# Kernel tuning notes

Measured on AMD Instinct MI355X. Metric: run time of the kernel, lower is better.

## Reference

```python
import jax, jax.numpy as jnp
import numpy as np

# Model dims (match init_kwargs)
B, S, D = 4, 2048, 1024          # batch, seq, d_model
H, E, DH = 8, 4, 128             # n_heads, n_experts_attn, d_head
K = 2                            # k_attn (routed, n_expert_shared_attn=0)
NEG_INF = jnp.float32(-1e30)


def setup_inputs() -> dict:
    key = jax.random.key(0)
    ks = jax.random.split(key, 9)
    s = np.float32(1.0 / np.sqrt(D))
    return {
        "q_src": jax.random.normal(ks[0], (B, S, D), jnp.float32),
        "k_src": jax.random.normal(ks[1], (B, S, D), jnp.float32),
        "v_src": jax.random.normal(ks[2], (B, S, D), jnp.float32),
        "wq": jax.random.normal(ks[3], (H * DH, D), jnp.float32) * s,
        "wk": jax.random.normal(ks[4], (H * DH, D), jnp.float32) * s,
        "sel_v_w": jax.random.normal(ks[5], (H * E, D), jnp.float32) * s,
        "sel_o_w": jax.random.normal(ks[6], (H * E, D), jnp.float32) * s,
        "v_w": jax.random.normal(ks[7], (H, E, D, DH), jnp.float32) * s,
        "o_w": jax.random.normal(ks[8], (H, E, DH, D), jnp.float32) * np.float32(1.0 / np.sqrt(H * DH)),
        "bias_v": jnp.zeros((E,), jnp.float32),   # load-balancing bias buffer (zeros at init)
        "bias_o": jnp.zeros((E,), jnp.float32),
        # causal boolean mask, True = attend (skip_mask all True -> trimming is identity)
        "attn_mask": jnp.broadcast_to(jnp.tril(jnp.ones((S, S), bool)), (B, S, S)),
        "position_ids": jnp.broadcast_to(jnp.arange(S, dtype=jnp.int32), (B, S)),
        "skip_mask": jnp.ones((B, S), bool),
    }


def _expert_gate(x, w, bias):
    """Sigmoid gating + per-head top-k routed expert selection.
    Returns dense combine weights [b,s,h,E] (sum of sel_val * one_hot) and indices [b,s,h,K]."""
    logits = (x @ w.T).reshape(*x.shape[:-1], H, E)        # [b,s,h,E]
    sel = jax.nn.sigmoid(logits)
    # bias only affects *which* experts are picked (added under no_grad in torch)
    _, idx = jax.lax.top_k(jax.lax.stop_gradient(sel) + bias, K)  # [b,s,h,K]
    sel_val = jnp.take_along_axis(sel, idx, axis=-1)        # [b,s,h,K]
    gate = jnp.sum(jax.nn.one_hot(idx, E, dtype=sel.dtype) * sel_val[..., None], axis=-2)
    return gate, idx


def reference(q_src, k_src, v_src, wq, wk, sel_v_w, sel_o_w, v_w, o_w,
              bias_v, bias_o, attn_mask, position_ids, skip_mask):
    # scale.sqrt() applied to both q and k -> full 1/sqrt(d_head) on scores
    ssq = jnp.float32((1.0 / np.sqrt(DH)) ** 0.5)
    q = ((q_src @ wq.T) * ssq).reshape(B, S, H, DH).transpose(0, 2, 1, 3)  # [b,h,s,dh]
    k = ((k_src @ wk.T) * ssq).reshape(B, S, H, DH).transpose(0, 2, 1, 3)

    v_gate, v_idx = _expert_gate(k_src, sel_v_w, bias_v)    # V experts routed on k_src
    o_gate, o_idx = _expert_gate(q_src, sel_o_w, bias_o)    # O experts routed on q_src

    # expert-mixed V projection (cvmm): all experts then dense combine
    all_v = jnp.einsum('bsm,hemd->bshed', v_src, v_w)       # [b,s,h,E,dh]
    v = jnp.einsum('bshed,bshe->bhsd', all_v, v_gate)       # [b,h,s,dh]

    scores = jnp.einsum('bhqd,bhkd->bhqk', q, k)
    scores = jnp.where(attn_mask[:, None], scores, NEG_INF)
    attn = jax.nn.softmax(scores, axis=-1)
    out = jnp.einsum('bhqk,bhkd->bqhd', attn, v)            # [b,s,h,dh]

    # expert-mixed O projection, summed over heads
    scaled = out[..., None, :] * o_gate[..., None]          # [b,s,h,E,dh]
    res = jnp.einsum('bshed,hedm->bsm', scaled, o_w)        # [b,s,d_model]
    return res, (v_idx, o_idx)
```

## Files before the change

kernel.cpp:

```cpp
#include <hip/hip_runtime.h>
#include <cstdint>
#include <cstddef>

typedef __bf16 bf16;
typedef __bf16 bf16x4 __attribute__((ext_vector_type(4)));
typedef __bf16 bf16x8 __attribute__((ext_vector_type(8)));
typedef float  fx4    __attribute__((ext_vector_type(4)));


__device__ __forceinline__ void async16(const void* g, void* l) {
  __builtin_amdgcn_global_load_lds((const __attribute__((address_space(1))) void*)g,
                                   (__attribute__((address_space(3))) void*)l, 16, 0, 0);
}

#define BARRIER() do { asm volatile("" ::: "memory"); __builtin_amdgcn_s_barrier(); \
                       asm volatile("" ::: "memory"); } while (0)

template <int CTRL>
__device__ __forceinline__ float dppf(float x) {
  return __int_as_float(__builtin_amdgcn_update_dpp(
      0, __float_as_int(x), CTRL, 0xf, 0xf, true));
}

__global__ __launch_bounds__(256) void f32_to_bf16(const float4* __restrict__ src,
                                                   bf16x4* __restrict__ dst, int n4) {
  int i = blockIdx.x * 256 + threadIdx.x;
  if (i < n4) {
    float4 v = src[i];
    bf16x4 o;
    o[0] = (bf16)v.x; o[1] = (bf16)v.y; o[2] = (bf16)v.z; o[3] = (bf16)v.w;
    dst[i] = o;
  }
}

__global__ __launch_bounds__(256) void make_wvt(const float* __restrict__ v_w,
                                                bf16* __restrict__ wvt) {
  __shared__ float tile[64][65];
  const int he = blockIdx.z, k0 = blockIdx.x * 64, dh0 = blockIdx.y * 64;
  const float* in = v_w + (size_t)he * 1024 * 128;
  #pragma unroll
  for (int j = 0; j < 16; j++) {
    int idx = threadIdx.x + j * 256;
    int r = idx >> 6, c = idx & 63;
    tile[r][c] = in[(size_t)(k0 + r) * 128 + dh0 + c];
  }
  __syncthreads();
  const int h = he >> 2, e = he & 3;
  bf16* outp = wvt + ((size_t)(h * 128 + dh0) * 4 + e) * 1024 + k0;
  #pragma unroll
  for (int j = 0; j < 16; j++) {
    int idx = threadIdx.x + j * 256;
    int r = idx >> 6, c = idx & 63;
    outp[(size_t)r * 4096 + c] = (bf16)tile[c][r];
  }
}

__global__ __launch_bounds__(256) void make_wot(const float* __restrict__ o_w,
                                                bf16* __restrict__ wot) {
  __shared__ float tile[64][65];
  const int he = blockIdx.z, d0 = blockIdx.x * 64, dh0 = blockIdx.y * 64;
  const float* in = o_w + (size_t)he * 128 * 1024;
  #pragma unroll
  for (int j = 0; j < 16; j++) {
    int idx = threadIdx.x + j * 256;
    int r = idx >> 6, c = idx & 63;
    tile[r][c] = in[(size_t)(dh0 + r) * 1024 + d0 + c];
  }
  __syncthreads();
  bf16* outp = wot + (size_t)d0 * 4096 + he * 128 + dh0;
  #pragma unroll
  for (int j = 0; j < 16; j++) {
    int idx = threadIdx.x + j * 256;
    int r = idx >> 6, c = idx & 63;
    outp[(size_t)r * 4096 + c] = (bf16)tile[c][r];
  }
}

__global__ __launch_bounds__(256) void gating(const float* __restrict__ q_src,
                                              const float* __restrict__ k_src,
                                              const float* __restrict__ sel_v_w,
                                              const float* __restrict__ sel_o_w,
                                              const float* __restrict__ bias_v,
                                              const float* __restrict__ bias_o,
                                              float* __restrict__ gate_v,
                                              float* __restrict__ gate_o,
                                              float* __restrict__ d_out) {
  const int g = blockIdx.y;
  const int m0 = blockIdx.x * 64;
  const float* x = g ? q_src : k_src;
  const float* w = g ? sel_o_w : sel_v_w;
  const float* bias = g ? bias_o : bias_v;
  float* gate = g ? gate_o : gate_v;
  float* idxo = d_out + 8388608 + g * 131072;

  __shared__ __align__(16) float smem[2 * 12288];

  const int t = threadIdx.x;
  const int hg = t & 7;
  const int tg = t >> 3;

  auto stage = [&](int buf, int k0) {
    float* xs = smem + buf * 12288;
    float* ws = xs + 8192;
    #pragma unroll
    for (int p = 0; p < 8; p++) {
      int of = p * 1024 + t * 4;
      int row = of >> 7, c = (of >> 2) & 31;
      int sc = c ^ ((row >> 1) & 7);
      async16(x + (size_t)(m0 + row) * 1024 + k0 + sc * 4, xs + of);
    }
    #pragma unroll
    for (int p = 0; p < 4; p++) {
      int of = p * 1024 + t * 4;
      int row = of >> 7, c = (of >> 2) & 31;
      int sc = c ^ ((row >> 2) & 7);
      async16(w + (size_t)row * 1024 + k0 + sc * 4, ws + of);
    }
  };

  double acc[2][4] = {};

  stage(0, 0);
  int buf = 0;
  for (int c8 = 0; c8 < 8; c8++) {
    if (c8 < 7) {
      stage(buf ^ 1, (c8 + 1) * 128);
      asm volatile("s_waitcnt vmcnt(12)" ::: "memory");
    } else {
      asm volatile("s_waitcnt vmcnt(0)" ::: "memory");
    }
    BARRIER();
    const float* xs = smem + buf * 12288;
    const float* ws = xs + 8192;
    const int xr0 = tg * 2;
    #pragma unroll 4
    for (int k4 = 0; k4 < 32; k4++) {
      float4 x0 = *(const float4*)(xs + (size_t)xr0 * 128 + (size_t)((k4 ^ (tg & 7)) * 4));
      float4 x1 = *(const float4*)(xs + (size_t)(xr0 + 1) * 128 + (size_t)((k4 ^ (tg & 7)) * 4));
      double x0d[4] = {(double)x0.x, (double)x0.y, (double)x0.z, (double)x0.w};
      double x1d[4] = {(double)x1.x, (double)x1.y, (double)x1.z, (double)x1.w};
      #pragma unroll
      for (int e = 0; e < 4; e++) {
        int wr = hg * 4 + e;
        float4 wv = *(const float4*)(ws + (size_t)wr * 128 + (size_t)((k4 ^ hg) * 4));
        double w0 = (double)wv.x, w1 = (double)wv.y, w2 = (double)wv.z, w3 = (double)wv.w;
        acc[0][e] += x0d[0] * w0 + x0d[1] * w1 + x0d[2] * w2 + x0d[3] * w3;
        acc[1][e] += x1d[0] * w0 + x1d[1] * w1 + x1d[2] * w2 + x1d[3] * w3;
      }
    }
    BARRIER();
    buf ^= 1;
  }

  const float log2e = 1.4426950408889634f;
  float b0 = bias[0], b1 = bias[1], b2 = bias[2], b3 = bias[3];
  #pragma unroll
  for (int tok = 0; tok < 2; tok++) {
    int m = m0 + tg * 2 + tok;
    float sel[4];
    #pragma unroll
    for (int e = 0; e < 4; e++) {
      float lv = (float)acc[tok][e];
      sel[e] = 1.0f / (1.0f + __builtin_amdgcn_exp2f(-lv * log2e));
    }
    float vb[4] = {sel[0] + b0, sel[1] + b1, sel[2] + b2, sel[3] + b3};
    int i0 = 0;
    #pragma unroll
    for (int e = 1; e < 4; e++) if (vb[e] > vb[i0]) i0 = e;
    int i1 = -1; float best = -1e30f;
    #pragma unroll
    for (int e = 0; e < 4; e++) { if (e == i0) continue; if (vb[e] > best) { best = vb[e]; i1 = e; } }
    float4 gv;
    gv.x = (i0 == 0 || i1 == 0) ? sel[0] : 0.f;
    gv.y = (i0 == 1 || i1 == 1) ? sel[1] : 0.f;
    gv.z = (i0 == 2 || i1 == 2) ? sel[2] : 0.f;
    gv.w = (i0 == 3 || i1 == 3) ? sel[3] : 0.f;
    *(float4*)(gate + ((size_t)m * 8 + hg) * 4) = gv;
    idxo[m * 16 + hg * 2 + 0] = (float)i0;
    idxo[m * 16 + hg * 2 + 1] = (float)i1;
  }
}

__global__ __launch_bounds__(256) void expand_o(const bf16* __restrict__ outb,
                                                const float* __restrict__ gate_o,
                                                bf16* __restrict__ Ae) {
  int idx = blockIdx.x * 256 + threadIdx.x;
  int m = idx >> 9;
  int u = idx & 511;
  int he = u >> 4;
  int hh = he >> 2, e = he & 3;
  int dh0 = (u & 15) * 8;
  float gv = gate_o[((size_t)m * 8 + hh) * 4 + e];
  bf16x8 v = *(const bf16x8*)(outb + ((size_t)m * 8 + hh) * 128 + dh0);
  #pragma unroll
  for (int j = 0; j < 8; j++) v[j] = (bf16)((float)v[j] * gv);
  *(bf16x8*)(Ae + (size_t)m * 4096 + u * 8) = v;
}

template <int MODE>
__global__ __launch_bounds__(512) void gemm_moe(const bf16* __restrict__ Abf,
                                                const bf16* __restrict__ BT,
                                                const float* __restrict__ gate,
                                                bf16* __restrict__ Cbf,
                                                float* __restrict__ Cf32,
                                                float scale) {
  constexpr int KDIM = (MODE == 0) ? 1024 : 4096;
  constexpr int ASTRIDE = (MODE == 2) ? 4096 : 1024;
  __shared__ __align__(16) bf16 smem[49152];
  const int t = threadIdx.x;
  const int wave = t >> 6, lane = t & 63;
  const int wr = wave >> 1, wc = wave & 1;
  const int quad = lane >> 4, l16 = lane & 15;
  const int bid = blockIdx.x;
  const int m0 = (bid >> 3) * 256;
  const int n0 = (MODE == 1) ? 0 : (bid & 7) * 128;
  const int h = (MODE == 1) ? (bid & 7) : 0;
  const bf16* BTh = (MODE == 1) ? BT + (size_t)h * 128 * 4096 : BT;

  fx4 acc[4][4] = {};
  fx4 accT[4][4] = {};

  const int srow = t >> 3, sch = t & 7;

  auto stage = [&](int buf, int k0) {
    bf16* As = smem + buf * 16384;
    bf16* Bs = smem + 32768 + buf * 8192;
    #pragma unroll
    for (int p = 0; p < 2; p++) {
      int row = p * 64 + srow;
      int sc = sch ^ (row & 7);
      async16(BTh + (size_t)(n0 + row) * KDIM + k0 + sc * 8,
              Bs + row * 64 + sch * 8);
    }
    int col = (MODE == 1) ? (k0 & 1023) : k0;
    #pragma unroll
    for (int p = 0; p < 4; p++) {
      int row = p * 64 + srow;
      int sc = sch ^ (row & 7);
      async16(Abf + (size_t)(m0 + row) * ASTRIDE + col + sc * 8,
              As + row * 64 + sch * 8);
    }
  };

  stage(0, 0);
  int buf = 0;
  for (int k0 = 0; k0 < KDIM; k0 += 64) {
    if (k0 + 64 < KDIM) {
      stage(buf ^ 1, k0 + 64);
      asm volatile("s_waitcnt vmcnt(6)" ::: "memory");
    } else {
      asm volatile("s_waitcnt vmcnt(0)" ::: "memory");
    }
    BARRIER();
    const bf16* As = smem + buf * 16384;
    const bf16* Bs = smem + 32768 + buf * 8192;
    #pragma unroll
    for (int kk = 0; kk < 64; kk += 32) {
      bf16x8 af[4], bfr[4];
      #pragma unroll
      for (int i = 0; i < 4; i++) {
        int ar = wr * 64 + i * 16 + l16;
        af[i] = *(const bf16x8*)(As + ar * 64 + ((((kk >> 3) + quad) ^ (ar & 7)) * 8));
      }
      #pragma unroll
      for (int i = 0; i < 2; i++) {
        int br = wc * 64 + i * 16 + l16;
        bfr[i] = *(const bf16x8*)(Bs + br * 64 + ((((kk >> 3) + quad) ^ (br & 7)) * 8));
      }
      BARRIER();
      __builtin_amdgcn_s_setprio(1);
      #pragma unroll
      for (int mi = 0; mi < 4; mi++)
        #pragma unroll
        for (int ni = 0; ni < 2; ni++)
          acc[mi][ni] = __builtin_amdgcn_mfma_f32_16x16x32_bf16(af[mi], bfr[ni], acc[mi][ni], 0, 0, 0);
      __builtin_amdgcn_s_setprio(0);
      BARRIER();
      #pragma unroll
      for (int i = 2; i < 4; i++) {
        int br = wc * 64 + i * 16 + l16;
        bfr[i] = *(const bf16x8*)(Bs + br * 64 + ((((kk >> 3) + quad) ^ (br & 7)) * 8));
      }
      BARRIER();
      __builtin_amdgcn_s_setprio(1);
      #pragma unroll
      for (int mi = 0; mi < 4; mi++)
        #pragma unroll
        for (int ni = 2; ni < 4; ni++)
          acc[mi][ni] = __builtin_amdgcn_mfma_f32_16x16x32_bf16(af[mi], bfr[ni], acc[mi][ni], 0, 0, 0);
      __builtin_amdgcn_s_setprio(0);
      BARRIER();
    }
    if constexpr (MODE == 1) {
      if (((k0 + 64) & 1023) == 0) {
        const int e = k0 >> 10;
        #pragma unroll
        for (int mi = 0; mi < 4; mi++)
          #pragma unroll
          for (int r = 0; r < 4; r++) {
            int m = m0 + wr * 64 + mi * 16 + quad * 4 + r;
            float gv = gate[((size_t)m * 8 + h) * 4 + e];
            #pragma unroll
            for (int ni = 0; ni < 4; ni++)
              accT[mi][ni][r] += gv * acc[mi][ni][r];
          }
        #pragma unroll
        for (int mi = 0; mi < 4; mi++)
          #pragma unroll
          for (int ni = 0; ni < 4; ni++)
            #pragma unroll
            for (int j = 0; j < 4; j++) acc[mi][ni][j] = 0.f;
      }
    }
    buf ^= 1;
  }

  if (MODE == 1) {
    #pragma unroll
    for (int mi = 0; mi < 4; mi++)
      #pragma unroll
      for (int ni = 0; ni < 4; ni++) {
        int nl = wc * 64 + ni * 16 + l16;
        int ml = wr * 64 + mi * 16 + quad * 4;
        bf16x4 pk;
        #pragma unroll
        for (int r = 0; r < 4; r++) pk[r] = (bf16)accT[mi][ni][r];
        *(bf16x4*)(smem + nl * 264 + ml) = pk;
      }
    __syncthreads();
    int b = m0 >> 11, s0 = m0 & 2047;
    const int row = t >> 2, seg = t & 3;
    bf16* dst = Cbf + (((size_t)(b * 8 + h) * 128) + row) * 2048 + s0 + seg * 64;
    #pragma unroll
    for (int j = 0; j < 8; j++)
      *(float4*)(dst + j * 8) = *(float4*)(smem + row * 264 + seg * 64 + j * 8);
    return;
  }

  #pragma unroll
  for (int mi = 0; mi < 4; mi++)
    #pragma unroll
    for (int ni = 0; ni < 4; ni++)
      #pragma unroll
      for (int r = 0; r < 4; r++) {
        int m = m0 + wr * 64 + mi * 16 + quad * 4 + r;
        int n = n0 + wc * 64 + ni * 16 + l16;
        float v = acc[mi][ni][r] * scale;
        if (MODE == 0) {
          int b = m >> 11, s = m & 2047, hh = n >> 7, dh = n & 127;
          Cbf[(((size_t)(b * 8 + hh) * 2048 + s) << 7) + dh] = (bf16)v;
        } else {
          Cf32[(size_t)m * 1024 + n] = v;
        }
      }
}

__global__ __launch_bounds__(256) void attn_kernel(const bf16* __restrict__ qb,
                                                   const bf16* __restrict__ kb,
                                                   const bf16* __restrict__ vbT,
                                                   bf16* __restrict__ outb) {
  const int bh = blockIdx.y;
  const int b = bh >> 3, h = bh & 7;
  __shared__ __align__(16) bf16 Ks[2][64 * 128];
  __shared__ __align__(16) bf16 VTs[2][128 * 64];
  __shared__ __align__(16) bf16 Ps[4][16][72];
  const int t = threadIdx.x, wave = t >> 6, lane = t & 63;
  const int quad = lane >> 4, l16 = lane & 15;
  const bf16* qbase  = qb  + (size_t)bh * 2048 * 128;
  const bf16* kbase  = kb  + (size_t)bh * 2048 * 128;
  const bf16* vtbase = vbT + (size_t)bh * 128 * 2048;

  auto stage = [&](int buf, int kt) {
    #pragma unroll
    for (int p = 0; p < 4; p++) {
      int o = p * 4096 + wave * 1024 + lane * 16;
      int kr = o >> 8, kc = o & 255;
      async16((const char*)kbase + (size_t)(kt * 64 + kr) * 256 + (kc ^ ((kr & 7) << 4)),
              (char*)&Ks[buf][0] + o);
    }
    #pragma unroll
    for (int p = 0; p < 4; p++) {
      int o = p * 4096 + wave * 1024 + lane * 16;
      int vr = o >> 7, vc = o & 127;
      async16((const char*)vtbase + (size_t)vr * 4096 + kt * 128 + (vc ^ ((vr & 7) << 4)),
              (char*)&VTs[buf][0] + o);
    }
  };

  #pragma unroll 1
  for (int pass = 0; pass < 2; pass++) {
    const int qt = pass ? blockIdx.x : (31 - blockIdx.x);

    bf16x8 qf[4];
    #pragma unroll
    for (int dk = 0; dk < 4; dk++)
      qf[dk] = *(const bf16x8*)(qbase + (size_t)(qt * 64 + wave * 16 + l16) * 128 + dk * 32 + quad * 8);

    float m_run[4], l_run[4];
    fx4 acc_o[8] = {};
    #pragma unroll
    for (int r = 0; r < 4; r++) { m_run[r] = -1e30f; l_run[r] = 0.f; }

    stage(0, 0);
    int cur = 0;

    for (int kt = 0; kt <= qt; kt++) {
      if (kt < qt) {
        stage(cur ^ 1, kt + 1);
        asm volatile("s_waitcnt vmcnt(8)" ::: "memory");
      } else {
        asm volatile("s_waitcnt vmcnt(0)" ::: "memory");
      }
      __builtin_amdgcn_s_barrier();
      asm volatile("" ::: "memory");

      const char* Ksb  = (const char*)&Ks[cur][0];
      const char* VTsb = (const char*)&VTs[cur][0];

      fx4 accs[4] = {};
      __builtin_amdgcn_s_setprio(1);
      #pragma unroll
      for (int ni = 0; ni < 4; ni++)
        #pragma unroll
        for (int dk = 0; dk < 4; dk++) {
          int r = ni * 16 + l16;
          bf16x8 kf = *(const bf16x8*)(Ksb + r * 256 + ((dk * 64 + quad * 16) ^ ((r & 7) << 4)));
          accs[ni] = __builtin_amdgcn_mfma_f32_16x16x32_bf16(qf[dk], kf, accs[ni], 0, 0, 0);
        }
      __builtin_amdgcn_s_setprio(0);

      if (kt == qt) {
        #pragma unroll
        for (int ni = 0; ni < 4; ni++)
          #pragma unroll
          for (int r = 0; r < 4; r++) {
            int qr = wave * 16 + quad * 4 + r;
            int kc = ni * 16 + l16;
            if (kc > qr) accs[ni][r] = -1e30f;
          }
      }

      #pragma unroll
      for (int r = 0; r < 4; r++) {
        float mx = fmaxf(fmaxf(accs[0][r], accs[1][r]), fmaxf(accs[2][r], accs[3][r]));
        mx = fmaxf(mx, dppf<0x121>(mx));
        mx = fmaxf(mx, dppf<0x122>(mx));
        mx = fmaxf(mx, dppf<0x124>(mx));
        mx = fmaxf(mx, dppf<0x128>(mx));
        float m_new = fmaxf(m_run[r], mx);
        float alpha = __builtin_amdgcn_exp2f(m_run[r] - m_new);
        float rs = 0.f;
        #pragma unroll
        for (int ni = 0; ni < 4; ni++) {
          float p = __builtin_amdgcn_exp2f(accs[ni][r] - m_new);
          accs[ni][r] = p; rs += p;
        }
        rs += dppf<0x121>(rs);
        rs += dppf<0x122>(rs);
        rs += dppf<0x124>(rs);
        rs += dppf<0x128>(rs);
        l_run[r] = l_run[r] * alpha + rs;
        m_run[r] = m_new;
        #pragma unroll
        for (int nj = 0; nj < 8; nj++) acc_o[nj][r] *= alpha;
      }

      #pragma unroll
      for (int ni = 0; ni < 4; ni++)
        #pragma unroll
        for (int r = 0; r < 4; r++)
          Ps[wave][quad * 4 + r][ni * 16 + l16] = (bf16)accs[ni][r];

      __builtin_amdgcn_s_setprio(1);
      #pragma unroll
      for (int step = 0; step < 2; step++) {
        bf16x8 pf = *(const bf16x8*)&Ps[wave][l16][step * 32 + quad * 8];
        #pragma unroll
        for (int nj = 0; nj < 8; nj++) {
          int r = nj * 16 + l16;
          bf16x8 vf = *(const bf16x8*)(VTsb + r * 128 + ((step * 64 + quad * 16) ^ ((r & 7) << 4)));
          acc_o[nj] = __builtin_amdgcn_mfma_f32_16x16x32_bf16(pf, vf, acc_o[nj], 0, 0, 0);
        }
      }
      __builtin_amdgcn_s_setprio(0);

      asm volatile("" ::: "memory");
      __builtin_amdgcn_s_barrier();
      cur ^= 1;
    }

    #pragma unroll
    for (int nj = 0; nj < 8; nj++)
      #pragma unroll
      for (int r = 0; r < 4; r++) {
        int s = qt * 64 + wave * 16 + quad * 4 + r;
        int token = b * 2048 + s;
        float o = acc_o[nj][r] / l_run[r];
        outb[((size_t)token * 8 + h) * 128 + nj * 16 + l16] = (bf16)o;
      }
  }
}

extern "C" void kernel_launch(void* const* d_in, const int* in_sizes, int n_in,
                              void* d_out, int out_size, void* d_ws, size_t ws_size,
                              hipStream_t stream) {
  const float* q_src  = (const float*)d_in[0];
  const float* k_src  = (const float*)d_in[1];
  const float* v_src  = (const float*)d_in[2];
  const float* wq     = (const float*)d_in[3];
  const float* wk     = (const float*)d_in[4];
  const float* sel_v_w = (const float*)d_in[5];
  const float* sel_o_w = (const float*)d_in[6];
  const float* v_w    = (const float*)d_in[7];
  const float* o_w    = (const float*)d_in[8];
  const float* bias_v = (const float*)d_in[9];
  const float* bias_o = (const float*)d_in[10];
  float* out = (float*)d_out;

  char* ws = (char*)d_ws;
  size_t off = 0;
  auto alloc = [&](size_t bytes) { char* p = ws + off; off += (bytes + 255) & ~(size_t)255; return p; };
  bf16* wqb   = (bf16*)alloc((size_t)1024 * 1024 * 2);
  bf16* wkb   = (bf16*)alloc((size_t)1024 * 1024 * 2);
  bf16* wvt   = (bf16*)alloc((size_t)8 * 128 * 4 * 1024 * 2);
  bf16* wot   = (bf16*)alloc((size_t)1024 * 4096 * 2);
  float* gate_v = (float*)alloc((size_t)8192 * 32 * 4);
  float* gate_o = (float*)alloc((size_t)8192 * 32 * 4);
  bf16* qsb   = (bf16*)alloc((size_t)8192 * 1024 * 2);
  bf16* ksb   = (bf16*)alloc((size_t)8192 * 1024 * 2);
  bf16* vsb   = (bf16*)alloc((size_t)8192 * 1024 * 2);
  bf16* qb    = (bf16*)alloc((size_t)8192 * 1024 * 2);
  bf16* kb    = (bf16*)alloc((size_t)8192 * 1024 * 2);
  bf16* vbT   = (bf16*)alloc((size_t)8192 * 1024 * 2);
  bf16* outb  = (bf16*)alloc((size_t)8192 * 1024 * 2);
  bf16* Ae    = qsb;

  f32_to_bf16<<<1024, 256, 0, stream>>>((const float4*)wq, (bf16x4*)wqb, 262144);
  f32_to_bf16<<<1024, 256, 0, stream>>>((const float4*)wk, (bf16x4*)wkb, 262144);
  f32_to_bf16<<<8192, 256, 0, stream>>>((const float4*)q_src, (bf16x4*)qsb, 2097152);
  f32_to_bf16<<<8192, 256, 0, stream>>>((const float4*)k_src, (bf16x4*)ksb, 2097152);
  f32_to_bf16<<<8192, 256, 0, stream>>>((const float4*)v_src, (bf16x4*)vsb, 2097152);
  make_wvt<<<dim3(16, 2, 32), 256, 0, stream>>>(v_w, wvt);
  make_wot<<<dim3(16, 2, 32), 256, 0, stream>>>(o_w, wot);
  gating<<<dim3(128, 2), 256, 0, stream>>>(q_src, k_src, sel_v_w, sel_o_w,
                                           bias_v, bias_o, gate_v, gate_o, out);

  const float ssq = 0.29730177875068026f;
  const float log2e = 1.4426950408889634f;
  gemm_moe<0><<<256, 512, 0, stream>>>(qsb, wqb, nullptr, qb, nullptr, ssq * log2e);
  gemm_moe<0><<<256, 512, 0, stream>>>(ksb, wkb, nullptr, kb, nullptr, ssq);
  gemm_moe<1><<<256, 512, 0, stream>>>(vsb, wvt, gate_v, vbT, nullptr, 1.0f);
  attn_kernel<<<dim3(16, 32), 256, 0, stream>>>(qb, kb, vbT, outb);
  expand_o<<<16384, 256, 0, stream>>>(outb, gate_o, Ae);
  gemm_moe<2><<<256, 512, 0, stream>>>(Ae, wot, nullptr, nullptr, out, 1.0f);
}
```

Measured before the change: 597.4 us.

## Use two waves per attention block, each handling 32 query rows

```diff
diff --git a/kernel.cpp b/kernel.cpp
--- a/kernel.cpp
+++ b/kernel.cpp
@@ -355,15 +355,17 @@
       }
 }
 
-__global__ __launch_bounds__(256) void attn_kernel(const bf16* __restrict__ qb,
+__global__ __launch_bounds__(128) void attn_kernel(const bf16* __restrict__ qb,
                                                    const bf16* __restrict__ kb,
                                                    const bf16* __restrict__ vbT,
                                                    bf16* __restrict__ outb) {
-  const int bh = blockIdx.y;
+  const int linear = blockIdx.y * 16 + blockIdx.x;
+  const int bh = (linear & 7) * 4 + ((linear >> 3) & 3);
+  const int px = linear >> 5;
   const int b = bh >> 3, h = bh & 7;
   __shared__ __align__(16) bf16 Ks[2][64 * 128];
   __shared__ __align__(16) bf16 VTs[2][128 * 64];
-  __shared__ __align__(16) bf16 Ps[4][16][72];
+  __shared__ __align__(16) bf16 Ps[2][32][72];
   const int t = threadIdx.x, wave = t >> 6, lane = t & 63;
   const int quad = lane >> 4, l16 = lane & 15;
   const bf16* qbase  = qb  + (size_t)bh * 2048 * 128;
@@ -372,15 +374,15 @@
 
   auto stage = [&](int buf, int kt) {
     #pragma unroll
-    for (int p = 0; p < 4; p++) {
-      int o = p * 4096 + wave * 1024 + lane * 16;
+    for (int p = 0; p < 8; p++) {
+      int o = p * 2048 + t * 16;
       int kr = o >> 8, kc = o & 255;
       async16((const char*)kbase + (size_t)(kt * 64 + kr) * 256 + (kc ^ ((kr & 7) << 4)),
               (char*)&Ks[buf][0] + o);
     }
     #pragma unroll
-    for (int p = 0; p < 4; p++) {
-      int o = p * 4096 + wave * 1024 + lane * 16;
+    for (int p = 0; p < 8; p++) {
+      int o = p * 2048 + t * 16;
       int vr = o >> 7, vc = o & 127;
       async16((const char*)vtbase + (size_t)vr * 4096 + kt * 128 + (vc ^ ((vr & 7) << 4)),
               (char*)&VTs[buf][0] + o);
@@ -389,17 +391,22 @@
 
   #pragma unroll 1
   for (int pass = 0; pass < 2; pass++) {
-    const int qt = pass ? blockIdx.x : (31 - blockIdx.x);
-
-    bf16x8 qf[4];
-    #pragma unroll
-    for (int dk = 0; dk < 4; dk++)
-      qf[dk] = *(const bf16x8*)(qbase + (size_t)(qt * 64 + wave * 16 + l16) * 128 + dk * 32 + quad * 8);
-
-    float m_run[4], l_run[4];
-    fx4 acc_o[8] = {};
-    #pragma unroll
-    for (int r = 0; r < 4; r++) { m_run[r] = -1e30f; l_run[r] = 0.f; }
+    const int qt = pass ? px : (31 - px);
+
+    bf16x8 qf[2][4];
+    #pragma unroll
+    for (int g = 0; g < 2; g++)
+      #pragma unroll
+      for (int dk = 0; dk < 4; dk++)
+        qf[g][dk] = *(const bf16x8*)(qbase +
+            (size_t)(qt * 64 + wave * 32 + g * 16 + l16) * 128 + dk * 32 + quad * 8);
+
+    float m_run[2][4], l_run[2][4];
+    fx4 acc_o[2][8] = {};
+    #pragma unroll
+    for (int g = 0; g < 2; g++)
+      #pragma unroll
+      for (int r = 0; r < 4; r++) { m_run[g][r] = -1e30f; l_run[g][r] = 0.f; }
 
     stage(0, 0);
     int cur = 0;
@@ -407,7 +414,7 @@
     for (int kt = 0; kt <= qt; kt++) {
       if (kt < qt) {
         stage(cur ^ 1, kt + 1);
-        asm volatile("s_waitcnt vmcnt(8)" ::: "memory");
+        asm volatile("s_waitcnt vmcnt(16)" ::: "memory");
       } else {
         asm volatile("s_waitcnt vmcnt(0)" ::: "memory");
       }
@@ -417,7 +424,7 @@
       const char* Ksb  = (const char*)&Ks[cur][0];
       const char* VTsb = (const char*)&VTs[cur][0];
 
-      fx4 accs[4] = {};
+      fx4 accs[2][4] = {};
       __builtin_amdgcn_s_setprio(1);
       #pragma unroll
       for (int ni = 0; ni < 4; ni++)
@@ -425,61 +432,71 @@
         for (int dk = 0; dk < 4; dk++) {
           int r = ni * 16 + l16;
           bf16x8 kf = *(const bf16x8*)(Ksb + r * 256 + ((dk * 64 + quad * 16) ^ ((r & 7) << 4)));
-          accs[ni] = __builtin_amdgcn_mfma_f32_16x16x32_bf16(qf[dk], kf, accs[ni], 0, 0, 0);
+          accs[0][ni] = __builtin_amdgcn_mfma_f32_16x16x32_bf16(qf[0][dk], kf, accs[0][ni], 0, 0, 0);
+          accs[1][ni] = __builtin_amdgcn_mfma_f32_16x16x32_bf16(qf[1][dk], kf, accs[1][ni], 0, 0, 0);
         }
       __builtin_amdgcn_s_setprio(0);
 
       if (kt == qt) {
         #pragma unroll
+        for (int g = 0; g < 2; g++)
+          #pragma unroll
+          for (int ni = 0; ni < 4; ni++)
+            #pragma unroll
+            for (int r = 0; r < 4; r++) {
+              int qr = wave * 32 + g * 16 + quad * 4 + r;
+              int kc = ni * 16 + l16;
+              if (kc > qr) accs[g][ni][r] = -1e30f;
+            }
+      }
+
+      #pragma unroll
+      for (int g = 0; g < 2; g++)
+        #pragma unroll
+        for (int r = 0; r < 4; r++) {
+          float mx = fmaxf(fmaxf(accs[g][0][r], accs[g][1][r]),
+                           fmaxf(accs[g][2][r], accs[g][3][r]));
+          mx = fmaxf(mx, dppf<0x121>(mx));
+          mx = fmaxf(mx, dppf<0x122>(mx));
+          mx = fmaxf(mx, dppf<0x124>(mx));
+          mx = fmaxf(mx, dppf<0x128>(mx));
+          float m_new = fmaxf(m_run[g][r], mx);
+          float alpha = __builtin_amdgcn_exp2f(m_run[g][r] - m_new);
+          float rs = 0.f;
+          #pragma unroll
+          for (int ni = 0; ni < 4; ni++) {
+            float p = __builtin_amdgcn_exp2f(accs[g][ni][r] - m_new);
+            accs[g][ni][r] = p; rs += p;
+          }
+          rs += dppf<0x121>(rs);
+          rs += dppf<0x122>(rs);
+          rs += dppf<0x124>(rs);
+          rs += dppf<0x128>(rs);
+          l_run[g][r] = l_run[g][r] * alpha + rs;
+          m_run[g][r] = m_new;
+          #pragma unroll
+          for (int nj = 0; nj < 8; nj++) acc_o[g][nj][r] *= alpha;
+        }
+
+      #pragma unroll
+      for (int g = 0; g < 2; g++)
+        #pragma unroll
         for (int ni = 0; ni < 4; ni++)
           #pragma unroll
-          for (int r = 0; r < 4; r++) {
-            int qr = wave * 16 + quad * 4 + r;
-            int kc = ni * 16 + l16;
-            if (kc > qr) accs[ni][r] = -1e30f;
-          }
-      }
-
-      #pragma unroll
-      for (int r = 0; r < 4; r++) {
-        float mx = fmaxf(fmaxf(accs[0][r], accs[1][r]), fmaxf(accs[2][r], accs[3][r]));
-        mx = fmaxf(mx, dppf<0x121>(mx));
-        mx = fmaxf(mx, dppf<0x122>(mx));
-        mx = fmaxf(mx, dppf<0x124>(mx));
-        mx = fmaxf(mx, dppf<0x128>(mx));
-        float m_new = fmaxf(m_run[r], mx);
-        float alpha = __builtin_amdgcn_exp2f(m_run[r] - m_new);
-        float rs = 0.f;
-        #pragma unroll
-        for (int ni = 0; ni < 4; ni++) {
-          float p = __builtin_amdgcn_exp2f(accs[ni][r] - m_new);
-          accs[ni][r] = p; rs += p;
-        }
-        rs += dppf<0x121>(rs);
-        rs += dppf<0x122>(rs);
-        rs += dppf<0x124>(rs);
-        rs += dppf<0x128>(rs);
-        l_run[r] = l_run[r] * alpha + rs;
-        m_run[r] = m_new;
-        #pragma unroll
-        for (int nj = 0; nj < 8; nj++) acc_o[nj][r] *= alpha;
-      }
-
-      #pragma unroll
-      for (int ni = 0; ni < 4; ni++)
-        #pragma unroll
-        for (int r = 0; r < 4; r++)
-          Ps[wave][quad * 4 + r][ni * 16 + l16] = (bf16)accs[ni][r];
+          for (int r = 0; r < 4; r++)
+            Ps[wave][g * 16 + quad * 4 + r][ni * 16 + l16] = (bf16)accs[g][ni][r];
 
       __builtin_amdgcn_s_setprio(1);
       #pragma unroll
       for (int step = 0; step < 2; step++) {
-        bf16x8 pf = *(const bf16x8*)&Ps[wave][l16][step * 32 + quad * 8];
+        bf16x8 pf0 = *(const bf16x8*)&Ps[wave][l16][step * 32 + quad * 8];
+        bf16x8 pf1 = *(const bf16x8*)&Ps[wave][16 + l16][step * 32 + quad * 8];
         #pragma unroll
         for (int nj = 0; nj < 8; nj++) {
           int r = nj * 16 + l16;
           bf16x8 vf = *(const bf16x8*)(VTsb + r * 128 + ((step * 64 + quad * 16) ^ ((r & 7) << 4)));
-          acc_o[nj] = __builtin_amdgcn_mfma_f32_16x16x32_bf16(pf, vf, acc_o[nj], 0, 0, 0);
+          acc_o[0][nj] = __builtin_amdgcn_mfma_f32_16x16x32_bf16(pf0, vf, acc_o[0][nj], 0, 0, 0);
+          acc_o[1][nj] = __builtin_amdgcn_mfma_f32_16x16x32_bf16(pf1, vf, acc_o[1][nj], 0, 0, 0);
         }
       }
       __builtin_amdgcn_s_setprio(0);
@@ -490,14 +507,16 @@
     }
 
     #pragma unroll
-    for (int nj = 0; nj < 8; nj++)
-      #pragma unroll
-      for (int r = 0; r < 4; r++) {
-        int s = qt * 64 + wave * 16 + quad * 4 + r;
-        int token = b * 2048 + s;
-        float o = acc_o[nj][r] / l_run[r];
-        outb[((size_t)token * 8 + h) * 128 + nj * 16 + l16] = (bf16)o;
-      }
+    for (int g = 0; g < 2; g++)
+      #pragma unroll
+      for (int nj = 0; nj < 8; nj++)
+        #pragma unroll
+        for (int r = 0; r < 4; r++) {
+          int s = qt * 64 + wave * 32 + g * 16 + quad * 4 + r;
+          int token = b * 2048 + s;
+          float o = acc_o[g][nj][r] / l_run[g][r];
+          outb[((size_t)token * 8 + h) * 128 + nj * 16 + l16] = (bf16)o;
+        }
   }
 }
 
@@ -550,7 +569,7 @@
   gemm_moe<0><<<256, 512, 0, stream>>>(qsb, wqb, nullptr, qb, nullptr, ssq * log2e);
   gemm_moe<0><<<256, 512, 0, stream>>>(ksb, wkb, nullptr, kb, nullptr, ssq);
   gemm_moe<1><<<256, 512, 0, stream>>>(vsb, wvt, gate_v, vbT, nullptr, 1.0f);
-  attn_kernel<<<dim3(16, 32), 256, 0, stream>>>(qb, kb, vbT, outb);
+  attn_kernel<<<dim3(16, 32), 128, 0, stream>>>(qb, kb, vbT, outb);
   expand_o<<<16384, 256, 0, stream>>>(outb, gate_o, Ae);
   gemm_moe<2><<<256, 512, 0, stream>>>(Ae, wot, nullptr, nullptr, out, 1.0f);
 }
```

After: 613.8 us. 1.03x slower.
